# Kernel optimization log

Hardware: AMD Instinct MI355X
Metric: run time of the kernel (lower is better)

The kernel has to match this reference:

```python
import jax, jax.numpy as jnp
from jax import lax
import numpy as np

C, C_MID, K_ENC, K_UP, SCALE = 128, 64, 3, 5, 2
B, H, W = 4, 48, 48
BN_EPS = 1e-3  # ultralytics Conv BN eps
EPS = 1e-6


def setup_inputs() -> dict:
    key = jax.random.key(0)
    ks = jax.random.split(key, 12)
    n_enc = (SCALE * K_UP) ** 2  # 100
    return {
        "x": jax.random.uniform(ks[0], (B, C, H, W), dtype=jnp.float32),
        "comp_w": jax.random.normal(ks[1], (C_MID, C, 1, 1), dtype=jnp.float32) * 0.05,
        "comp_bn_g": jax.random.normal(ks[2], (C_MID,), dtype=jnp.float32) * 0.1 + 1.0,
        "comp_bn_b": jax.random.normal(ks[3], (C_MID,), dtype=jnp.float32) * 0.1,
        "comp_bn_m": jax.random.normal(ks[4], (C_MID,), dtype=jnp.float32) * 0.1,
        "comp_bn_v": jax.random.uniform(ks[5], (C_MID,), dtype=jnp.float32, minval=0.5, maxval=1.5),
        "enc_w": jax.random.normal(ks[6], (n_enc, C_MID, K_ENC, K_ENC), dtype=jnp.float32) * 0.05,
        "enc_bn_g": jax.random.normal(ks[7], (n_enc,), dtype=jnp.float32) * 0.1 + 1.0,
        "enc_bn_b": jax.random.normal(ks[8], (n_enc,), dtype=jnp.float32) * 0.1,
        "enc_bn_m": jax.random.normal(ks[9], (n_enc,), dtype=jnp.float32) * 0.1,
        "enc_bn_v": jax.random.uniform(ks[10], (n_enc,), dtype=jnp.float32, minval=0.5, maxval=1.5),
    }


def _conv_bn(x, w, g, b, m, v, pad, act):
    y = lax.conv_general_dilated(
        x, w, window_strides=(1, 1), padding=[(pad, pad), (pad, pad)],
        dimension_numbers=("NCHW", "OIHW", "NCHW"))
    scale = (g * lax.rsqrt(v + BN_EPS))[None, :, None, None]
    y = (y - m[None, :, None, None]) * scale + b[None, :, None, None]
    if act:  # SiLU
        y = y * jax.nn.sigmoid(y)
    return y


def reference(x, comp_w, comp_bn_g, comp_bn_b, comp_bn_m, comp_bn_v,
              enc_w, enc_bn_g, enc_bn_b, enc_bn_m, enc_bn_v):
    b, c, h, w = x.shape
    h_, w_ = h * SCALE, w * SCALE

    # ---- SAGamma: self-adaptive gamma correction ----
    gray = 0.299 * x[:, 0] + 0.587 * x[:, 1] + 0.114 * x[:, 2]  # (b,h,w)
    gm = jnp.mean(gray, axis=(1, 2), keepdims=True)              # (b,1,1)
    gs = jnp.std(gray, axis=(1, 2), ddof=1, keepdims=True)       # unbiased, like torch
    gamma = 0.8 + (1.2 - 0.8) * gm / (gm + jnp.maximum(gs, EPS))
    gamma = jnp.clip(gamma, 0.8, 1.2)[:, None]                   # (b,1,1,1)
    x = jnp.power(x + EPS, gamma)

    # ---- CARAFE ----
    # kernel prediction: comp (1x1 Conv+BN+SiLU) -> enc (3x3 Conv+BN, no act)
    Wk = _conv_bn(x, comp_w, comp_bn_g, comp_bn_b, comp_bn_m, comp_bn_v, pad=0, act=True)
    Wk = _conv_bn(Wk, enc_w, enc_bn_g, enc_bn_b, enc_bn_m, enc_bn_v, pad=K_ENC // 2, act=False)
    # pixel shuffle: (b, 25*s*s, h, w) -> (b, 25, h_, w_)
    k2 = K_UP * K_UP
    Wk = Wk.reshape(b, k2, SCALE, SCALE, h, w)
    Wk = Wk.transpose(0, 1, 4, 2, 5, 3).reshape(b, k2, h_, w_)
    Wk = jax.nn.softmax(Wk, axis=1)

    # nearest upsample x2
    Xu = jnp.repeat(jnp.repeat(x, SCALE, axis=2), SCALE, axis=3)  # (b,c,h_,w_)
    # unfold with kernel 5, dilation 2, pad 4 -> (b,c,25,h_,w_), torch (c,kh,kw) ordering
    pad = (K_UP // 2) * SCALE
    Xp = jnp.pad(Xu, ((0, 0), (0, 0), (pad, pad), (pad, pad)))
    patches = jnp.stack(
        [Xp[:, :, i * SCALE:i * SCALE + h_, j * SCALE:j * SCALE + w_]
         for i in range(K_UP) for j in range(K_UP)], axis=2)      # (b,c,25,h_,w_)

    return jnp.einsum("bkhw,bckhw->bchw", Wk, patches)
```

## Files before the change

kernel.cpp:

```cpp
#include <hip/hip_runtime.h>
#include <hip/hip_bf16.h>
#include <math.h>

#define CB   128
#define CMID 64
#define NENC 100
#define HH   48
#define WW   48
#define BB   4
#define HW   (HH*WW)
#define H2   (HH*2)
#define W2   (WW*2)
#define PS   56
#define PROWS 50
#define PCOL0 4
#define PLANE (PROWS*PS)
#define Y1P_FLOATS (BB*CMID*PLANE)

__global__ void zero_kernel(float4* __restrict__ p, int n4) {
    int idx = blockIdx.x * blockDim.x + threadIdx.x;
    if (idx < n4) p[idx] = make_float4(0.f, 0.f, 0.f, 0.f);
}

__global__ void gamma_kernel(const float* __restrict__ x, float* __restrict__ gamma) {
    int b = blockIdx.x;
    const float* xb = x + (size_t)b * CB * HW;
    const float4* R4 = (const float4*)xb;
    const float4* G4 = (const float4*)(xb + HW);
    const float4* B4 = (const float4*)(xb + 2 * HW);
    float s = 0.f, s2 = 0.f;
    for (int i = threadIdx.x; i < HW / 4; i += blockDim.x) {
        float4 r = R4[i], g = G4[i], bl = B4[i];
        float g0 = 0.299f * r.x + 0.587f * g.x + 0.114f * bl.x;
        float g1 = 0.299f * r.y + 0.587f * g.y + 0.114f * bl.y;
        float g2 = 0.299f * r.z + 0.587f * g.z + 0.114f * bl.z;
        float g3 = 0.299f * r.w + 0.587f * g.w + 0.114f * bl.w;
        s  += (g0 + g1) + (g2 + g3);
        s2 += (g0 * g0 + g1 * g1) + (g2 * g2 + g3 * g3);
    }
    for (int o = 32; o > 0; o >>= 1) {
        s  += __shfl_down(s, o);
        s2 += __shfl_down(s2, o);
    }
    __shared__ float ss[4], ss2[4];
    int wid = threadIdx.x >> 6;
    if ((threadIdx.x & 63) == 0) { ss[wid] = s; ss2[wid] = s2; }
    __syncthreads();
    if (threadIdx.x == 0) {
        float S = 0.f, S2 = 0.f;
        int nw = blockDim.x >> 6;
        for (int i = 0; i < nw; i++) { S += ss[i]; S2 += ss2[i]; }
        const float N = (float)HW;
        float gm = S / N;
        float var = (S2 - S * S / N) / (N - 1.0f);
        var = fmaxf(var, 0.f);
        float gs = sqrtf(var);
        float gam = 0.8f + 0.4f * gm / (gm + fmaxf(gs, 1e-6f));
        gam = fminf(fmaxf(gam, 0.8f), 1.2f);
        gamma[b] = gam;
    }
}

__global__ void pow_kernel(const float* __restrict__ x, const float* __restrict__ gamma,
                           float* __restrict__ xg) {
    int idx = blockIdx.x * blockDim.x + threadIdx.x;
    const int total4 = BB * CB * HW / 4;
    if (idx >= total4) return;
    int b = idx / (CB * HW / 4);
    float gam = gamma[b];
    float4 xv = ((const float4*)x)[idx];
    float4 r;
    r.x = powf(xv.x + 1e-6f, gam);
    r.y = powf(xv.y + 1e-6f, gam);
    r.z = powf(xv.z + 1e-6f, gam);
    r.w = powf(xv.w + 1e-6f, gam);
    ((float4*)xg)[idx] = r;
}

__global__ void conv1_kernel(const float* __restrict__ xg, const float* __restrict__ w,
                             const float* __restrict__ g, const float* __restrict__ bta,
                             const float* __restrict__ m, const float* __restrict__ vv,
                             float* __restrict__ y1p) {
    int idx = blockIdx.x * blockDim.x + threadIdx.x;
    const int PG = HW / 4;
    const int total = BB * CMID * PG;
    if (idx >= total) return;
    int pg = idx % PG;
    int cm = (idx / PG) % CMID;
    int b  = idx / (CMID * PG);
    const float4* xb = (const float4*)(xg + (size_t)b * CB * HW) + pg;
    const float* wc = w + cm * CB;
    float4 acc = {0.f, 0.f, 0.f, 0.f};
#pragma unroll 8
    for (int c = 0; c < CB; c++) {
        float4 xv = xb[(size_t)c * PG];
        float wv = wc[c];
        acc.x = fmaf(wv, xv.x, acc.x);
        acc.y = fmaf(wv, xv.y, acc.y);
        acc.z = fmaf(wv, xv.z, acc.z);
        acc.w = fmaf(wv, xv.w, acc.w);
    }
    float sc = g[cm] * rsqrtf(vv[cm] + 1e-3f);
    float sh = bta[cm] - m[cm] * sc;
    float4 o;
    float t;
    t = acc.x * sc + sh; o.x = t / (1.f + expf(-t));
    t = acc.y * sc + sh; o.y = t / (1.f + expf(-t));
    t = acc.z * sc + sh; o.z = t / (1.f + expf(-t));
    t = acc.w * sc + sh; o.w = t / (1.f + expf(-t));
    int row = pg / 12, col = (pg % 12) * 4;
    float* dst = y1p + ((size_t)(b * CMID + cm)) * PLANE + (row + 1) * PS + (col + PCOL0);
    *(float4*)dst = o;
}

__global__ __launch_bounds__(192) void conv3_kernel(
        const float* __restrict__ y1p, const float* __restrict__ w,
        const float* __restrict__ g, const float* __restrict__ bta,
        const float* __restrict__ m, const float* __restrict__ vv,
        float* __restrict__ wk2) {
    int blk = blockIdx.x;
    int e   = blk % NENC;
    int tmp = blk / NENC;
    int rb  = tmp % 3, b = tmp / 3;
    int t   = threadIdx.x;
    int row = rb * 16 + t / 12;
    int c0  = (t % 12) * 4;
    const float* wbase = w + (size_t)e * CMID * 9;
    const float* yb = y1p + (size_t)b * CMID * PLANE + row * PS + (c0 + PCOL0);

    float acc0 = 0.f, acc1 = 0.f, acc2 = 0.f, acc3 = 0.f;

    float  lf0 = yb[-1];          float4 m0 = *(const float4*)yb;            float rt0 = yb[4];
    float  lf1 = yb[PS - 1];      float4 m1 = *(const float4*)(yb + PS);     float rt1 = yb[PS + 4];
    float  lf2 = yb[2*PS - 1];    float4 m2 = *(const float4*)(yb + 2*PS);   float rt2 = yb[2*PS + 4];
    float w00 = wbase[0], w01 = wbase[1], w02 = wbase[2];
    float w10 = wbase[3], w11 = wbase[4], w12 = wbase[5];
    float w20 = wbase[6], w21 = wbase[7], w22 = wbase[8];

    for (int cm = 0; cm < CMID - 1; ++cm) {
        const float* yn = yb + (size_t)(cm + 1) * PLANE;
        float  nlf0 = yn[-1];        float4 nm0 = *(const float4*)yn;          float nrt0 = yn[4];
        float  nlf1 = yn[PS - 1];    float4 nm1 = *(const float4*)(yn + PS);   float nrt1 = yn[PS + 4];
        float  nlf2 = yn[2*PS - 1];  float4 nm2 = *(const float4*)(yn + 2*PS); float nrt2 = yn[2*PS + 4];
        const float* wn = wbase + (cm + 1) * 9;
        float nw00 = wn[0], nw01 = wn[1], nw02 = wn[2];
        float nw10 = wn[3], nw11 = wn[4], nw12 = wn[5];
        float nw20 = wn[6], nw21 = wn[7], nw22 = wn[8];

        acc0 = fmaf(w00, lf0,  fmaf(w01, m0.x, fmaf(w02, m0.y, acc0)));
        acc1 = fmaf(w00, m0.x, fmaf(w01, m0.y, fmaf(w02, m0.z, acc1)));
        acc2 = fmaf(w00, m0.y, fmaf(w01, m0.z, fmaf(w02, m0.w, acc2)));
        acc3 = fmaf(w00, m0.z, fmaf(w01, m0.w, fmaf(w02, rt0,  acc3)));
        acc0 = fmaf(w10, lf1,  fmaf(w11, m1.x, fmaf(w12, m1.y, acc0)));
        acc1 = fmaf(w10, m1.x, fmaf(w11, m1.y, fmaf(w12, m1.z, acc1)));
        acc2 = fmaf(w10, m1.y, fmaf(w11, m1.z, fmaf(w12, m1.w, acc2)));
        acc3 = fmaf(w10, m1.z, fmaf(w11, m1.w, fmaf(w12, rt1,  acc3)));
        acc0 = fmaf(w20, lf2,  fmaf(w21, m2.x, fmaf(w22, m2.y, acc0)));
        acc1 = fmaf(w20, m2.x, fmaf(w21, m2.y, fmaf(w22, m2.z, acc1)));
        acc2 = fmaf(w20, m2.y, fmaf(w21, m2.z, fmaf(w22, m2.w, acc2)));
        acc3 = fmaf(w20, m2.z, fmaf(w21, m2.w, fmaf(w22, rt2,  acc3)));

        lf0 = nlf0; m0 = nm0; rt0 = nrt0;
        lf1 = nlf1; m1 = nm1; rt1 = nrt1;
        lf2 = nlf2; m2 = nm2; rt2 = nrt2;
        w00 = nw00; w01 = nw01; w02 = nw02;
        w10 = nw10; w11 = nw11; w12 = nw12;
        w20 = nw20; w21 = nw21; w22 = nw22;
    }
    acc0 = fmaf(w00, lf0,  fmaf(w01, m0.x, fmaf(w02, m0.y, acc0)));
    acc1 = fmaf(w00, m0.x, fmaf(w01, m0.y, fmaf(w02, m0.z, acc1)));
    acc2 = fmaf(w00, m0.y, fmaf(w01, m0.z, fmaf(w02, m0.w, acc2)));
    acc3 = fmaf(w00, m0.z, fmaf(w01, m0.w, fmaf(w02, rt0,  acc3)));
    acc0 = fmaf(w10, lf1,  fmaf(w11, m1.x, fmaf(w12, m1.y, acc0)));
    acc1 = fmaf(w10, m1.x, fmaf(w11, m1.y, fmaf(w12, m1.z, acc1)));
    acc2 = fmaf(w10, m1.y, fmaf(w11, m1.z, fmaf(w12, m1.w, acc2)));
    acc3 = fmaf(w10, m1.z, fmaf(w11, m1.w, fmaf(w12, rt1,  acc3)));
    acc0 = fmaf(w20, lf2,  fmaf(w21, m2.x, fmaf(w22, m2.y, acc0)));
    acc1 = fmaf(w20, m2.x, fmaf(w21, m2.y, fmaf(w22, m2.z, acc1)));
    acc2 = fmaf(w20, m2.y, fmaf(w21, m2.z, fmaf(w22, m2.w, acc2)));
    acc3 = fmaf(w20, m2.z, fmaf(w21, m2.w, fmaf(w22, rt2,  acc3)));

    float sc = g[e] * rsqrtf(vv[e] + 1e-3f);
    float sh = bta[e] - m[e] * sc;
    float4 o = {acc0 * sc + sh, acc1 * sc + sh, acc2 * sc + sh, acc3 * sc + sh};
    *(float4*)(wk2 + (size_t)(b * NENC + e) * HW + row * WW + c0) = o;
}

__global__ void softmax_kernel(const float* __restrict__ wk2, float* __restrict__ wsm) {
    int idx = blockIdx.x * blockDim.x + threadIdx.x;
    const int total = BB * H2 * W2;
    if (idx >= total) return;
    int Wp = idx % W2, Hp = (idx / W2) % H2, b = idx / (H2 * W2);
    int h = Hp >> 1, w = Wp >> 1;
    int off = 2 * (Hp & 1) + (Wp & 1);
    const float* base = wk2 + (size_t)b * NENC * HW + (size_t)off * HW + h * WW + w;
    float vals[25];
    float mx = -1e30f;
#pragma unroll
    for (int k = 0; k < 25; k++) {
        float tv = base[(size_t)(4 * k) * HW];
        vals[k] = tv; mx = fmaxf(mx, tv);
    }
    float sum = 0.f;
#pragma unroll
    for (int k = 0; k < 25; k++) { float e2 = expf(vals[k] - mx); vals[k] = e2; sum += e2; }
    float inv = 1.f / sum;
#pragma unroll
    for (int k = 0; k < 25; k++)
        wsm[((size_t)(b * 25 + k) * H2 + Hp) * W2 + Wp] = vals[k] * inv;
}

__global__ void gather_kernel(const float* __restrict__ xg, const float* __restrict__ wsm,
                              float* __restrict__ out) {
    int idx = blockIdx.x * blockDim.x + threadIdx.x;
    const int total = BB * CB * HW;
    if (idx >= total) return;
    int w = idx % WW;
    int h = (idx / WW) % HH;
    int c = (idx / HW) % CB;
    int b = idx / (CB * HW);
    const float* xb = xg + ((size_t)b * CB + c) * HW;
    float xv[25];
#pragma unroll
    for (int i = 0; i < 5; i++) {
        int hy = h + i - 2;
        bool hok = (hy >= 0) && (hy < HH);
#pragma unroll
        for (int j = 0; j < 5; j++) {
            int wx = w + j - 2;
            bool ok = hok && (wx >= 0) && (wx < WW);
            xv[i * 5 + j] = ok ? xb[hy * WW + wx] : 0.f;
        }
    }
    float a0 = 0.f, a1 = 0.f, a2 = 0.f, a3 = 0.f;
    const float* wb = wsm + (size_t)b * 25 * H2 * W2;
    int r0 = (2 * h) * W2 + 2 * w;
#pragma unroll
    for (int k = 0; k < 25; k++) {
        const float* wkp = wb + (size_t)k * H2 * W2;
        float2 w0 = *(const float2*)(wkp + r0);
        float2 w1 = *(const float2*)(wkp + r0 + W2);
        float xk = xv[k];
        a0 = fmaf(w0.x, xk, a0);
        a1 = fmaf(w0.y, xk, a1);
        a2 = fmaf(w1.x, xk, a2);
        a3 = fmaf(w1.y, xk, a3);
    }
    float* ob = out + (((size_t)b * CB + c) * H2 + 2 * h) * W2 + 2 * w;
    float2 s0 = {a0, a1};
    float2 s1 = {a2, a3};
    *(float2*)ob = s0;
    *(float2*)(ob + W2) = s1;
}

extern "C" void kernel_launch(void* const* d_in, const int* in_sizes, int n_in,
                              void* d_out, int out_size, void* d_ws, size_t ws_size,
                              hipStream_t stream) {
    const float* x       = (const float*)d_in[0];
    const float* comp_w  = (const float*)d_in[1];
    const float* comp_g  = (const float*)d_in[2];
    const float* comp_b  = (const float*)d_in[3];
    const float* comp_m  = (const float*)d_in[4];
    const float* comp_v  = (const float*)d_in[5];
    const float* enc_w   = (const float*)d_in[6];
    const float* enc_g   = (const float*)d_in[7];
    const float* enc_b   = (const float*)d_in[8];
    const float* enc_m   = (const float*)d_in[9];
    const float* enc_v   = (const float*)d_in[10];
    float* out = (float*)d_out;

    float* ws = (float*)d_ws;
    float* gamma = ws;
    float* xg    = ws + 64;
    float* wk2   = xg + (size_t)BB * CB * HW;
    float* y1p   = wk2 + (size_t)BB * NENC * HW;
    float* wsm   = y1p;

    {
        int n4 = Y1P_FLOATS / 4;
        zero_kernel<<<(n4 + 255) / 256, 256, 0, stream>>>((float4*)y1p, n4);
    }
    gamma_kernel<<<BB, 256, 0, stream>>>(x, gamma);
    {
        int total4 = BB * CB * HW / 4;
        pow_kernel<<<(total4 + 255) / 256, 256, 0, stream>>>(x, gamma, xg);
    }
    {
        int total = BB * CMID * (HW / 4);
        conv1_kernel<<<(total + 255) / 256, 256, 0, stream>>>(
            xg, comp_w, comp_g, comp_b, comp_m, comp_v, y1p);
    }
    conv3_kernel<<<BB * 3 * NENC, 192, 0, stream>>>(
        y1p, enc_w, enc_g, enc_b, enc_m, enc_v, wk2);
    {
        int total = BB * H2 * W2;
        softmax_kernel<<<(total + 255) / 256, 256, 0, stream>>>(wk2, wsm);
    }
    {
        int total = BB * CB * HW;
        gather_kernel<<<(total + 255) / 256, 256, 0, stream>>>(xg, wsm, out);
    }
}
```

Before: 191.5 us.

## Compute two encoder channels per conv3 block, zero only halo, use fast math

The 3x3 encoder conv now produces two output channels per thread. Each loaded input stencil is therefore reused for twice as many FMAs, and the block count drops by half. The full memset of the padded intermediate is replaced by a kernel that zeros only the halo border, since conv1 writes the interior. powf and expf in the pow, SiLU and softmax paths are swapped for __expf/__logf intrinsics, trading some accuracy for cheaper transcendentals.

```diff
diff --git a/kernel.cpp b/kernel.cpp
--- a/kernel.cpp
+++ b/kernel.cpp
@@ -15,11 +15,24 @@
 #define PROWS 50
 #define PCOL0 4
 #define PLANE (PROWS*PS)
-#define Y1P_FLOATS (BB*CMID*PLANE)
-
-__global__ void zero_kernel(float4* __restrict__ p, int n4) {
-    int idx = blockIdx.x * blockDim.x + threadIdx.x;
-    if (idx < n4) p[idx] = make_float4(0.f, 0.f, 0.f, 0.f);
+#define EG   2
+
+__global__ void halo_kernel(float* __restrict__ y1p) {
+    int idx = blockIdx.x * blockDim.x + threadIdx.x;
+    int plane = idx / 124;
+    int t = idx % 124;
+    float* p = y1p + (size_t)plane * PLANE;
+    float4 z = make_float4(0.f, 0.f, 0.f, 0.f);
+    if (t < 14) {
+        *(float4*)(p + t * 4) = z;
+    } else if (t < 28) {
+        *(float4*)(p + 49 * PS + (t - 14) * 4) = z;
+    } else {
+        int s = t - 28;
+        int r = 1 + (s >> 1);
+        int col = (s & 1) ? 52 : 0;
+        *(float4*)(p + r * PS + col) = z;
+    }
 }
 
 __global__ void gamma_kernel(const float* __restrict__ x, float* __restrict__ gamma) {
@@ -70,10 +83,10 @@
     float gam = gamma[b];
     float4 xv = ((const float4*)x)[idx];
     float4 r;
-    r.x = powf(xv.x + 1e-6f, gam);
-    r.y = powf(xv.y + 1e-6f, gam);
-    r.z = powf(xv.z + 1e-6f, gam);
-    r.w = powf(xv.w + 1e-6f, gam);
+    r.x = __expf(gam * __logf(xv.x + 1e-6f));
+    r.y = __expf(gam * __logf(xv.y + 1e-6f));
+    r.z = __expf(gam * __logf(xv.z + 1e-6f));
+    r.w = __expf(gam * __logf(xv.w + 1e-6f));
     ((float4*)xg)[idx] = r;
 }
 
@@ -104,14 +117,20 @@
     float sh = bta[cm] - m[cm] * sc;
     float4 o;
     float t;
-    t = acc.x * sc + sh; o.x = t / (1.f + expf(-t));
-    t = acc.y * sc + sh; o.y = t / (1.f + expf(-t));
-    t = acc.z * sc + sh; o.z = t / (1.f + expf(-t));
-    t = acc.w * sc + sh; o.w = t / (1.f + expf(-t));
+    t = acc.x * sc + sh; o.x = t / (1.f + __expf(-t));
+    t = acc.y * sc + sh; o.y = t / (1.f + __expf(-t));
+    t = acc.z * sc + sh; o.z = t / (1.f + __expf(-t));
+    t = acc.w * sc + sh; o.w = t / (1.f + __expf(-t));
     int row = pg / 12, col = (pg % 12) * 4;
     float* dst = y1p + ((size_t)(b * CMID + cm)) * PLANE + (row + 1) * PS + (col + PCOL0);
     *(float4*)dst = o;
 }
+
+#define FMA4(A0,A1,A2,A3, wa,wb,wc, lf,mm,rt) \
+    A0 = fmaf(wa, lf,   fmaf(wb, mm.x, fmaf(wc, mm.y, A0))); \
+    A1 = fmaf(wa, mm.x, fmaf(wb, mm.y, fmaf(wc, mm.z, A1))); \
+    A2 = fmaf(wa, mm.y, fmaf(wb, mm.z, fmaf(wc, mm.w, A2))); \
+    A3 = fmaf(wa, mm.z, fmaf(wb, mm.w, fmaf(wc, rt,   A3)));
 
 __global__ __launch_bounds__(192) void conv3_kernel(
         const float* __restrict__ y1p, const float* __restrict__ w,
@@ -119,71 +138,77 @@
         const float* __restrict__ m, const float* __restrict__ vv,
         float* __restrict__ wk2) {
     int blk = blockIdx.x;
-    int e   = blk % NENC;
-    int tmp = blk / NENC;
+    int eg  = blk % (NENC / EG);
+    int tmp = blk / (NENC / EG);
     int rb  = tmp % 3, b = tmp / 3;
+    int e0  = eg * EG;
     int t   = threadIdx.x;
     int row = rb * 16 + t / 12;
     int c0  = (t % 12) * 4;
-    const float* wbase = w + (size_t)e * CMID * 9;
+    const float* wb0 = w + (size_t)e0 * CMID * 9;
+    const float* wb1 = wb0 + CMID * 9;
     const float* yb = y1p + (size_t)b * CMID * PLANE + row * PS + (c0 + PCOL0);
 
-    float acc0 = 0.f, acc1 = 0.f, acc2 = 0.f, acc3 = 0.f;
-
-    float  lf0 = yb[-1];          float4 m0 = *(const float4*)yb;            float rt0 = yb[4];
-    float  lf1 = yb[PS - 1];      float4 m1 = *(const float4*)(yb + PS);     float rt1 = yb[PS + 4];
-    float  lf2 = yb[2*PS - 1];    float4 m2 = *(const float4*)(yb + 2*PS);   float rt2 = yb[2*PS + 4];
-    float w00 = wbase[0], w01 = wbase[1], w02 = wbase[2];
-    float w10 = wbase[3], w11 = wbase[4], w12 = wbase[5];
-    float w20 = wbase[6], w21 = wbase[7], w22 = wbase[8];
+    float a00 = 0.f, a01 = 0.f, a02 = 0.f, a03 = 0.f;
+    float a10 = 0.f, a11 = 0.f, a12 = 0.f, a13 = 0.f;
+
+    float  lf0 = yb[-1];        float4 m0 = *(const float4*)yb;          float rt0 = yb[4];
+    float  lf1 = yb[PS-1];      float4 m1 = *(const float4*)(yb+PS);     float rt1 = yb[PS+4];
+    float  lf2 = yb[2*PS-1];    float4 m2 = *(const float4*)(yb+2*PS);   float rt2 = yb[2*PS+4];
+    float u00 = wb0[0], u01 = wb0[1], u02 = wb0[2];
+    float u10 = wb0[3], u11 = wb0[4], u12 = wb0[5];
+    float u20 = wb0[6], u21 = wb0[7], u22 = wb0[8];
+    float v00 = wb1[0], v01 = wb1[1], v02 = wb1[2];
+    float v10 = wb1[3], v11 = wb1[4], v12 = wb1[5];
+    float v20 = wb1[6], v21 = wb1[7], v22 = wb1[8];
 
     for (int cm = 0; cm < CMID - 1; ++cm) {
         const float* yn = yb + (size_t)(cm + 1) * PLANE;
-        float  nlf0 = yn[-1];        float4 nm0 = *(const float4*)yn;          float nrt0 = yn[4];
-        float  nlf1 = yn[PS - 1];    float4 nm1 = *(const float4*)(yn + PS);   float nrt1 = yn[PS + 4];
-        float  nlf2 = yn[2*PS - 1];  float4 nm2 = *(const float4*)(yn + 2*PS); float nrt2 = yn[2*PS + 4];
-        const float* wn = wbase + (cm + 1) * 9;
-        float nw00 = wn[0], nw01 = wn[1], nw02 = wn[2];
-        float nw10 = wn[3], nw11 = wn[4], nw12 = wn[5];
-        float nw20 = wn[6], nw21 = wn[7], nw22 = wn[8];
-
-        acc0 = fmaf(w00, lf0,  fmaf(w01, m0.x, fmaf(w02, m0.y, acc0)));
-        acc1 = fmaf(w00, m0.x, fmaf(w01, m0.y, fmaf(w02, m0.z, acc1)));
-        acc2 = fmaf(w00, m0.y, fmaf(w01, m0.z, fmaf(w02, m0.w, acc2)));
-        acc3 = fmaf(w00, m0.z, fmaf(w01, m0.w, fmaf(w02, rt0,  acc3)));
-        acc0 = fmaf(w10, lf1,  fmaf(w11, m1.x, fmaf(w12, m1.y, acc0)));
-        acc1 = fmaf(w10, m1.x, fmaf(w11, m1.y, fmaf(w12, m1.z, acc1)));
-        acc2 = fmaf(w10, m1.y, fmaf(w11, m1.z, fmaf(w12, m1.w, acc2)));
-        acc3 = fmaf(w10, m1.z, fmaf(w11, m1.w, fmaf(w12, rt1,  acc3)));
-        acc0 = fmaf(w20, lf2,  fmaf(w21, m2.x, fmaf(w22, m2.y, acc0)));
-        acc1 = fmaf(w20, m2.x, fmaf(w21, m2.y, fmaf(w22, m2.z, acc1)));
-        acc2 = fmaf(w20, m2.y, fmaf(w21, m2.z, fmaf(w22, m2.w, acc2)));
-        acc3 = fmaf(w20, m2.z, fmaf(w21, m2.w, fmaf(w22, rt2,  acc3)));
+        float  nlf0 = yn[-1];       float4 nm0 = *(const float4*)yn;         float nrt0 = yn[4];
+        float  nlf1 = yn[PS-1];     float4 nm1 = *(const float4*)(yn+PS);    float nrt1 = yn[PS+4];
+        float  nlf2 = yn[2*PS-1];   float4 nm2 = *(const float4*)(yn+2*PS);  float nrt2 = yn[2*PS+4];
+        const float* wn0 = wb0 + (cm + 1) * 9;
+        const float* wn1 = wb1 + (cm + 1) * 9;
+        float nu00 = wn0[0], nu01 = wn0[1], nu02 = wn0[2];
+        float nu10 = wn0[3], nu11 = wn0[4], nu12 = wn0[5];
+        float nu20 = wn0[6], nu21 = wn0[7], nu22 = wn0[8];
+        float nv00 = wn1[0], nv01 = wn1[1], nv02 = wn1[2];
+        float nv10 = wn1[3], nv11 = wn1[4], nv12 = wn1[5];
+        float nv20 = wn1[6], nv21 = wn1[7], nv22 = wn1[8];
+
+        FMA4(a00,a01,a02,a03, u00,u01,u02, lf0,m0,rt0)
+        FMA4(a00,a01,a02,a03, u10,u11,u12, lf1,m1,rt1)
+        FMA4(a00,a01,a02,a03, u20,u21,u22, lf2,m2,rt2)
+        FMA4(a10,a11,a12,a13, v00,v01,v02, lf0,m0,rt0)
+        FMA4(a10,a11,a12,a13, v10,v11,v12, lf1,m1,rt1)
+        FMA4(a10,a11,a12,a13, v20,v21,v22, lf2,m2,rt2)
 
         lf0 = nlf0; m0 = nm0; rt0 = nrt0;
         lf1 = nlf1; m1 = nm1; rt1 = nrt1;
         lf2 = nlf2; m2 = nm2; rt2 = nrt2;
-        w00 = nw00; w01 = nw01; w02 = nw02;
-        w10 = nw10; w11 = nw11; w12 = nw12;
-        w20 = nw20; w21 = nw21; w22 = nw22;
-    }
-    acc0 = fmaf(w00, lf0,  fmaf(w01, m0.x, fmaf(w02, m0.y, acc0)));
-    acc1 = fmaf(w00, m0.x, fmaf(w01, m0.y, fmaf(w02, m0.z, acc1)));
-    acc2 = fmaf(w00, m0.y, fmaf(w01, m0.z, fmaf(w02, m0.w, acc2)));
-    acc3 = fmaf(w00, m0.z, fmaf(w01, m0.w, fmaf(w02, rt0,  acc3)));
-    acc0 = fmaf(w10, lf1,  fmaf(w11, m1.x, fmaf(w12, m1.y, acc0)));
-    acc1 = fmaf(w10, m1.x, fmaf(w11, m1.y, fmaf(w12, m1.z, acc1)));
-    acc2 = fmaf(w10, m1.y, fmaf(w11, m1.z, fmaf(w12, m1.w, acc2)));
-    acc3 = fmaf(w10, m1.z, fmaf(w11, m1.w, fmaf(w12, rt1,  acc3)));
-    acc0 = fmaf(w20, lf2,  fmaf(w21, m2.x, fmaf(w22, m2.y, acc0)));
-    acc1 = fmaf(w20, m2.x, fmaf(w21, m2.y, fmaf(w22, m2.z, acc1)));
-    acc2 = fmaf(w20, m2.y, fmaf(w21, m2.z, fmaf(w22, m2.w, acc2)));
-    acc3 = fmaf(w20, m2.z, fmaf(w21, m2.w, fmaf(w22, rt2,  acc3)));
-
-    float sc = g[e] * rsqrtf(vv[e] + 1e-3f);
-    float sh = bta[e] - m[e] * sc;
-    float4 o = {acc0 * sc + sh, acc1 * sc + sh, acc2 * sc + sh, acc3 * sc + sh};
-    *(float4*)(wk2 + (size_t)(b * NENC + e) * HW + row * WW + c0) = o;
+        u00 = nu00; u01 = nu01; u02 = nu02;
+        u10 = nu10; u11 = nu11; u12 = nu12;
+        u20 = nu20; u21 = nu21; u22 = nu22;
+        v00 = nv00; v01 = nv01; v02 = nv02;
+        v10 = nv10; v11 = nv11; v12 = nv12;
+        v20 = nv20; v21 = nv21; v22 = nv22;
+    }
+    FMA4(a00,a01,a02,a03, u00,u01,u02, lf0,m0,rt0)
+    FMA4(a00,a01,a02,a03, u10,u11,u12, lf1,m1,rt1)
+    FMA4(a00,a01,a02,a03, u20,u21,u22, lf2,m2,rt2)
+    FMA4(a10,a11,a12,a13, v00,v01,v02, lf0,m0,rt0)
+    FMA4(a10,a11,a12,a13, v10,v11,v12, lf1,m1,rt1)
+    FMA4(a10,a11,a12,a13, v20,v21,v22, lf2,m2,rt2)
+
+    float sc0 = g[e0] * rsqrtf(vv[e0] + 1e-3f);
+    float sh0 = bta[e0] - m[e0] * sc0;
+    float sc1 = g[e0+1] * rsqrtf(vv[e0+1] + 1e-3f);
+    float sh1 = bta[e0+1] - m[e0+1] * sc1;
+    float* op = wk2 + (size_t)(b * NENC + e0) * HW + row * WW + c0;
+    float4 o0 = {a00*sc0+sh0, a01*sc0+sh0, a02*sc0+sh0, a03*sc0+sh0};
+    float4 o1 = {a10*sc1+sh1, a11*sc1+sh1, a12*sc1+sh1, a13*sc1+sh1};
+    *(float4*)op = o0;
+    *(float4*)(op + HW) = o1;
 }
 
 __global__ void softmax_kernel(const float* __restrict__ wk2, float* __restrict__ wsm) {
@@ -203,7 +228,7 @@
     }
     float sum = 0.f;
 #pragma unroll
-    for (int k = 0; k < 25; k++) { float e2 = expf(vals[k] - mx); vals[k] = e2; sum += e2; }
+    for (int k = 0; k < 25; k++) { float e2 = __expf(vals[k] - mx); vals[k] = e2; sum += e2; }
     float inv = 1.f / sum;
 #pragma unroll
     for (int k = 0; k < 25; k++)
@@ -276,10 +301,7 @@
     float* y1p   = wk2 + (size_t)BB * NENC * HW;
     float* wsm   = y1p;
 
-    {
-        int n4 = Y1P_FLOATS / 4;
-        zero_kernel<<<(n4 + 255) / 256, 256, 0, stream>>>((float4*)y1p, n4);
-    }
+    halo_kernel<<<(BB * CMID * 124) / 256, 256, 0, stream>>>(y1p);
     gamma_kernel<<<BB, 256, 0, stream>>>(x, gamma);
     {
         int total4 = BB * CB * HW / 4;
@@ -290,7 +312,7 @@
         conv1_kernel<<<(total + 255) / 256, 256, 0, stream>>>(
             xg, comp_w, comp_g, comp_b, comp_m, comp_v, y1p);
     }
-    conv3_kernel<<<BB * 3 * NENC, 192, 0, stream>>>(
+    conv3_kernel<<<BB * 3 * (NENC / EG), 192, 0, stream>>>(
         y1p, enc_w, enc_g, enc_b, enc_m, enc_v, wk2);
     {
         int total = BB * H2 * W2;
```

Measured after the change: 172.6 us. 1.11x faster.
